# Kernel tuning notes

Measured on AMD Instinct MI355X. Metric: run time of the kernel, lower is better.

## Reference

```python
import jax, jax.numpy as jnp
import numpy as np

NUM_HEADS = 16
MEMORY_LR = 0.1


def setup_inputs() -> dict:
    key = jax.random.key(0)
    ks = jax.random.split(key, 5)
    B, S, D = 4, 4096, 1024
    x = jax.random.normal(ks[0], (B, S, D), dtype=jnp.float32)
    # torch init: randn * 0.01, shape (out_features, in_features)
    Wq = jax.random.normal(ks[1], (D, D), dtype=jnp.float32) * 0.01
    Wk = jax.random.normal(ks[2], (D, D), dtype=jnp.float32) * 0.01
    Wv = jax.random.normal(ks[3], (D, D), dtype=jnp.float32) * 0.01
    Wo = jax.random.normal(ks[4], (D, D), dtype=jnp.float32) * 0.01
    return {"x": x, "Wq": Wq, "Wk": Wk, "Wv": Wv, "Wo": Wo}


def reference(x, Wq, Wk, Wv, Wo):
    B, S, D = x.shape
    H = NUM_HEADS
    hd = D // H
    # Projections (torch Linear: y = x @ W^T). Pending self-mod updates
    # (immediate_update=False) never change W during forward -> plain matmul.
    Q = (x @ Wq.T).reshape(B, S, H, hd)
    K = (x @ Wk.T).reshape(B, S, H, hd)
    V = (x @ Wv.T).reshape(B, S, H, hd)
    # time-major for scan: [S, B, H, hd]
    Qt = jnp.transpose(Q, (1, 0, 2, 3))
    Kt = jnp.transpose(K, (1, 0, 2, 3))
    Vt = jnp.transpose(V, (1, 0, 2, 3))

    def step(M, qkv):
        q, k, v = qkv  # each [B, H, hd]
        v_pred = jnp.einsum('hdk,bhk->bhd', M, k)
        err = v - v_pred
        # torch computes the update under no_grad -> constant w.r.t. params
        upd = jax.lax.stop_gradient(jnp.einsum('bhd,bhk->hdk', err, k) / B)
        M_new = M + MEMORY_LR * upd
        out = jnp.einsum('hdk,bhk->bhd', M_new, q)
        return M_new, out

    M0 = jnp.zeros((H, hd, hd), dtype=x.dtype)  # memory buffer starts at zero
    _, outs = jax.lax.scan(step, M0, (Qt, Kt, Vt))  # outs: [S, B, H, hd]
    out = jnp.transpose(outs, (1, 0, 2, 3)).reshape(B, S, D)
    # dropout p=0.0 -> identity
    return out @ Wo.T
```

## Files before the change

### kernel.cpp

```cpp
#include <hip/hip_runtime.h>


typedef unsigned short u16;
typedef __attribute__((ext_vector_type(8))) short short8;
typedef __attribute__((ext_vector_type(4))) float f32x4;

#define B_ 4
#define S_ 4096
#define D_ 1024
#define H_ 16
#define CHUNK 16
#define NCHUNK 256
#define SUPW 16
#define NSUP 16
#define ETA 0.025f

__device__ __forceinline__ u16 f2bf(float f) {
  unsigned u = __builtin_bit_cast(unsigned, f);
  u += 0x7fffu + ((u >> 16) & 1u);
  return (u16)(u >> 16);
}
__device__ __forceinline__ float bf2f(u16 s) {
  unsigned u = ((unsigned)s) << 16;
  return __builtin_bit_cast(float, u);
}
__device__ __forceinline__ float ldv(float v) { return v; }
__device__ __forceinline__ float ldv(u16 v) { return bf2f(v); }
__device__ __forceinline__ void stv(float* p, float v) { *p = v; }
__device__ __forceinline__ void stv(u16* p, float v) { *p = f2bf(v); }

#define MFMA __builtin_amdgcn_mfma_f32_16x16x32_bf16

__device__ __forceinline__ void gload16(const void* g, void* l) {
  __builtin_amdgcn_global_load_lds(
      (__attribute__((address_space(1))) void*)g,
      (__attribute__((address_space(3))) void*)l, 16, 0, 0);
}

__global__ void cvt_hi_kernel(const float* __restrict__ x, u16* __restrict__ hi, int n4) {
  int i = blockIdx.x * blockDim.x + threadIdx.x;
  int stride = gridDim.x * blockDim.x;
  for (; i < n4; i += stride) {
    float4 v = ((const float4*)x)[i];
    ushort4 h;
    h.x = f2bf(v.x); h.y = f2bf(v.y); h.z = f2bf(v.z); h.w = f2bf(v.w);
    ((ushort4*)hi)[i] = h;
  }
}

__global__ void cvt_hi4_kernel(const float* __restrict__ a, const float* __restrict__ b,
                               const float* __restrict__ c, const float* __restrict__ d,
                               u16* __restrict__ o, int n4) {
  const float* src = (blockIdx.y == 0) ? a : (blockIdx.y == 1) ? b
                   : (blockIdx.y == 2) ? c : d;
  u16* dst = o + (size_t)blockIdx.y * 1048576u;
  int i = blockIdx.x * blockDim.x + threadIdx.x;
  int stride = gridDim.x * blockDim.x;
  for (; i < n4; i += stride) {
    float4 v = ((const float4*)src)[i];
    ushort4 h;
    h.x = f2bf(v.x); h.y = f2bf(v.y); h.z = f2bf(v.z); h.w = f2bf(v.w);
    ((ushort4*)dst)[i] = h;
  }
}

template<int BPRE, typename OutT>
__global__ __launch_bounds__(256) void gemm_axw(
    const u16* __restrict__ Ahg, const void* __restrict__ Bhp,
    OutT* __restrict__ C, int M, int N, int K) {
  __shared__ __align__(16) u16 Ahs[2][128][32];
  __shared__ __align__(16) u16 Bhs[2][128][32];
  const int tid = threadIdx.x, w = tid >> 6, lane = tid & 63;
  const int bm = blockIdx.x * 128, bn = blockIdx.y * 128;
  const int wm = (w >> 1) * 64, wn = (w & 1) * 64;
  const int fr = lane & 15, kb = lane >> 4;
  const int lrow = lane >> 2, lcol = (lane & 3) * 8;

  auto stage = [&](int buf, int k0) {
    {
      const size_t rb = (size_t)(bm + w * 32 + lrow) * K + k0 + lcol;
      gload16(Ahg + rb, &Ahs[buf][w * 32][0]);
      gload16(Ahg + rb + (size_t)16 * K, &Ahs[buf][w * 32 + 16][0]);
    }
    if constexpr (BPRE) {
      const u16* Bhg = (const u16*)Bhp;
      const size_t rb = (size_t)(bn + w * 32 + lrow) * K + k0 + lcol;
      gload16(Bhg + rb, &Bhs[buf][w * 32][0]);
      gload16(Bhg + rb + (size_t)16 * K, &Bhs[buf][w * 32 + 16][0]);
    } else {
      const float* Bm = (const float*)Bhp;
#pragma unroll
      for (int i2 = 0; i2 < 4; ++i2) {
        int e = tid + i2 * 256, r = e >> 3, sg = (e & 7) * 4;
        float4 v = *(const float4*)(&Bm[(size_t)(bn + r) * K + k0 + sg]);
        ushort4 hq;
        hq.x = f2bf(v.x); hq.y = f2bf(v.y); hq.z = f2bf(v.z); hq.w = f2bf(v.w);
        *(ushort4*)(&Bhs[buf][r][sg]) = hq;
      }
    }
  };
  auto compute = [&](int buf, f32x4 (*acc)[4]) {
    short8 ah[4], bh[4];
#pragma unroll
    for (int mi = 0; mi < 4; ++mi)
      ah[mi] = *(const short8*)(&Ahs[buf][wm + mi * 16 + fr][kb * 8]);
#pragma unroll
    for (int ni = 0; ni < 4; ++ni)
      bh[ni] = *(const short8*)(&Bhs[buf][wn + ni * 16 + fr][kb * 8]);
#pragma unroll
    for (int mi = 0; mi < 4; ++mi)
#pragma unroll
      for (int ni = 0; ni < 4; ++ni)
        acc[mi][ni] = MFMA(ah[mi], bh[ni], acc[mi][ni], 0, 0, 0);
  };

  f32x4 acc[4][4];
#pragma unroll
  for (int i = 0; i < 4; ++i)
#pragma unroll
    for (int j = 0; j < 4; ++j) acc[i][j] = (f32x4){0.f, 0.f, 0.f, 0.f};

  const int nt = K >> 5;
  stage(0, 0);
  asm volatile("s_waitcnt vmcnt(0)" ::: "memory");
  __syncthreads();
  int cur = 0;
  for (int t = 0; t < nt; ++t) {
    if (t + 1 < nt) stage(cur ^ 1, (t + 1) * 32);
    compute(cur, acc);
    asm volatile("s_waitcnt vmcnt(0)" ::: "memory");
    __syncthreads();
    cur ^= 1;
  }
  const int fc = lane & 15, fr4 = (lane >> 4) * 4;
#pragma unroll
  for (int mi = 0; mi < 4; ++mi)
#pragma unroll
    for (int ni = 0; ni < 4; ++ni) {
      int gm = bm + wm + mi * 16 + fr4;
      int gn = bn + wn + ni * 16 + fc;
#pragma unroll
      for (int rg = 0; rg < 4; ++rg)
        stv(&C[(size_t)(gm + rg) * N + gn], acc[mi][ni][rg]);
    }
}

template<typename PT>
__global__ __launch_bounds__(256) void phase1_kernel(
    float* __restrict__ Qg, const u16* __restrict__ Kg, u16* __restrict__ Vg,
    PT* __restrict__ Pg, PT* __restrict__ Rg) {
  __shared__ __align__(16) u16 Ks[64][72];
  __shared__ __align__(16) u16 KsT[64][72];
  __shared__ __align__(16) u16 Gh[64][72];
  __shared__ __align__(16) u16 Gl[64][72];
  __shared__ __align__(16) float Ut[64][68];
  __shared__ __align__(16) float Wt[64][68];

  const int c = blockIdx.x, h = blockIdx.y, tid = threadIdx.x;
  const int w = tid >> 6, lane = tid & 63;
  const int fr = lane & 15, kq = lane >> 4, orow = kq * 4;
  const int xr = 16 * w + fr;

  auto gidx = [&](int r, int d) -> size_t {
    return ((size_t)(r & 3) * S_ + (size_t)c * CHUNK + (r >> 2)) * D_ + h * 64 + d;
  };
  auto ldb = [&](const u16 (*M)[72], int row, int s) -> short8 {
    return *(const short8*)(&M[row][32 * s + 8 * kq]);
  };
  auto ldf = [&](const float (*M)[68], int row, int s, short8& hh, short8& ll) {
    const float* p = &M[row][32 * s + 8 * kq];
#pragma unroll
    for (int j = 0; j < 8; ++j) {
      float v = p[j];
      u16 hb = f2bf(v);
      hh[j] = (short)hb;
      ll[j] = (short)f2bf(v - bf2f(hb));
    }
  };
  auto ldfh = [&](const float (*M)[68], int row, int s) -> short8 {
    const float* p = &M[row][32 * s + 8 * kq];
    short8 hh;
#pragma unroll
    for (int j = 0; j < 8; ++j) hh[j] = (short)f2bf(p[j]);
    return hh;
  };

  for (int i = tid; i < 4096; i += 256) {
    int r = i >> 6, d = i & 63;
    size_t g = gidx(r, d);
    u16 kraw = Kg[g];
    Ks[r][d] = kraw;
    KsT[d][r] = kraw;
    Wt[d][r] = ETA * bf2f(kraw);
    Ut[d][r] = ETA * bf2f(Vg[g]);
  }
  __syncthreads();

  f32x4 gacc[4];
#pragma unroll
  for (int ni = 0; ni < 4; ++ni) gacc[ni] = (f32x4){0.f, 0.f, 0.f, 0.f};
  {
    short8 xf[2];
#pragma unroll
    for (int s = 0; s < 2; ++s) xf[s] = ldb(Ks, xr, s);
#pragma unroll
    for (int ni = 0; ni < 4; ++ni)
#pragma unroll
      for (int s = 0; s < 2; ++s)
        gacc[ni] = MFMA(xf[s], ldb(Ks, 16 * ni + fr, s), gacc[ni], 0, 0, 0);
  }

  float sreg[4][4];
  {
    short8 xh[2], xl[2];
#pragma unroll
    for (int s = 0; s < 2; ++s) {
      const float* qp = &Qg[gidx(xr, 32 * s + 8 * kq)];
#pragma unroll
      for (int j = 0; j < 8; ++j) {
        float v = qp[j];
        u16 hb = f2bf(v);
        xh[s][j] = (short)hb;
        xl[s][j] = (short)f2bf(v - bf2f(hb));
      }
    }
    f32x4 acc[4];
#pragma unroll
    for (int ni = 0; ni < 4; ++ni) acc[ni] = (f32x4){0.f, 0.f, 0.f, 0.f};
#pragma unroll
    for (int ni = 0; ni < 4; ++ni)
#pragma unroll
      for (int s = 0; s < 2; ++s) {
        short8 yf = ldb(Ks, 16 * ni + fr, s);
        acc[ni] = MFMA(xh[s], yf, acc[ni], 0, 0, 0);
        acc[ni] = MFMA(xl[s], yf, acc[ni], 0, 0, 0);
      }
#pragma unroll
    for (int ni = 0; ni < 4; ++ni)
#pragma unroll
      for (int rg = 0; rg < 4; ++rg) {
        int r = 16 * w + orow + rg, cc = 16 * ni + fr;
        sreg[ni][rg] = ((r >> 2) >= (cc >> 2)) ? acc[ni][rg] : 0.f;
      }
  }
  __syncthreads();

#pragma unroll
  for (int ni = 0; ni < 4; ++ni)
#pragma unroll
    for (int rg = 0; rg < 4; ++rg) {
      float v = -ETA * gacc[ni][rg];
      u16 hb = f2bf(v);
      u16 lb = f2bf(v - bf2f(hb));
      int rr = 16 * w + orow + rg, cc = 16 * ni + fr;
      bool low = (rr >> 2) > (cc >> 2);
      u16 hm = low ? hb : (u16)0, lm = low ? lb : (u16)0;
      Gh[rr][cc] = hm;
      Gl[rr][cc] = lm;
      Ks[cc][rr] = hm;
    }
  __syncthreads();

  {
    short8 uh[2], ul[2], wh[2], wl[2];
#pragma unroll
    for (int s = 0; s < 2; ++s) { ldf(Ut, xr, s, uh[s], ul[s]); ldf(Wt, xr, s, wh[s], wl[s]); }
    f32x4 aU[4], aW[4];
#pragma unroll
    for (int ni = 0; ni < 4; ++ni) { aU[ni] = (f32x4){0.f,0.f,0.f,0.f}; aW[ni] = (f32x4){0.f,0.f,0.f,0.f}; }
#pragma unroll
    for (int ni = 0; ni < 4; ++ni)
#pragma unroll
      for (int s = 0; s < 2; ++s) {
        short8 yh = ldb(Gh, 16 * ni + fr, s);
        short8 yl = ldb(Gl, 16 * ni + fr, s);
        aU[ni] = MFMA(uh[s], yh, aU[ni], 0, 0, 0);
        aU[ni] = MFMA(uh[s], yl, aU[ni], 0, 0, 0);
        aU[ni] = MFMA(ul[s], yh, aU[ni], 0, 0, 0);
        aW[ni] = MFMA(wh[s], yh, aW[ni], 0, 0, 0);
        aW[ni] = MFMA(wh[s], yl, aW[ni], 0, 0, 0);
        aW[ni] = MFMA(wl[s], yh, aW[ni], 0, 0, 0);
      }
#pragma unroll
    for (int ni = 0; ni < 4; ++ni)
#pragma unroll
      for (int rg = 0; rg < 4; ++rg) {
        Ut[16 * w + orow + rg][16 * ni + fr] += aU[ni][rg];
        Wt[16 * w + orow + rg][16 * ni + fr] += aW[ni][rg];
      }
  }
  auto appSf = [&](const u16 (*Np)[72]) {
    short8 xu[2], xw[2];
#pragma unroll
    for (int s = 0; s < 2; ++s) { xu[s] = ldfh(Ut, xr, s); xw[s] = ldfh(Wt, xr, s); }
    f32x4 aU[4], aW[4];
#pragma unroll
    for (int ni = 0; ni < 4; ++ni) { aU[ni] = (f32x4){0.f,0.f,0.f,0.f}; aW[ni] = (f32x4){0.f,0.f,0.f,0.f}; }
#pragma unroll
    for (int ni = 0; ni < 4; ++ni)
#pragma unroll
      for (int s = 0; s < 2; ++s) {
        short8 yf = ldb(Np, 16 * ni + fr, s);
        aU[ni] = MFMA(xu[s], yf, aU[ni], 0, 0, 0);
        aW[ni] = MFMA(xw[s], yf, aW[ni], 0, 0, 0);
      }
#pragma unroll
    for (int ni = 0; ni < 4; ++ni)
#pragma unroll
      for (int rg = 0; rg < 4; ++rg) {
        Ut[16 * w + orow + rg][16 * ni + fr] += aU[ni][rg];
        Wt[16 * w + orow + rg][16 * ni + fr] += aW[ni][rg];
      }
  };

  {
    f32x4 sq[4];
#pragma unroll
    for (int ni = 0; ni < 4; ++ni) sq[ni] = (f32x4){0.f, 0.f, 0.f, 0.f};
    short8 xh[2];
#pragma unroll
    for (int s = 0; s < 2; ++s) xh[s] = ldb(Gh, xr, s);
#pragma unroll
    for (int ni = 0; ni < 4; ++ni)
#pragma unroll
      for (int s = 0; s < 2; ++s)
        sq[ni] = MFMA(xh[s], ldb(Ks, 16 * ni + fr, s), sq[ni], 0, 0, 0);
    __syncthreads();
#pragma unroll
    for (int ni = 0; ni < 4; ++ni)
#pragma unroll
      for (int rg = 0; rg < 4; ++rg) {
        u16 b = f2bf(sq[ni][rg]);
        int rr = 16 * w + orow + rg, cc = 16 * ni + fr;
        Ks[rr][cc] = b;
        Gh[cc][rr] = b;
      }
  }
  __syncthreads();

  appSf(Ks);
  {
    f32x4 sq[4];
#pragma unroll
    for (int ni = 0; ni < 4; ++ni) sq[ni] = (f32x4){0.f, 0.f, 0.f, 0.f};
    short8 xf[2];
#pragma unroll
    for (int s = 0; s < 2; ++s) xf[s] = ldb(Ks, xr, s);
#pragma unroll
    for (int ni = 0; ni < 4; ++ni)
#pragma unroll
      for (int s = 0; s < 2; ++s)
        sq[ni] = MFMA(xf[s], ldb(Gh, 16 * ni + fr, s), sq[ni], 0, 0, 0);
    __syncthreads();
#pragma unroll
    for (int ni = 0; ni < 4; ++ni)
#pragma unroll
      for (int rg = 0; rg < 4; ++rg) {
        u16 b = f2bf(sq[ni][rg]);
        int rr = 16 * w + orow + rg, cc = 16 * ni + fr;
        Gl[rr][cc] = b;
        Ks[cc][rr] = b;
      }
  }
  __syncthreads();

  appSf(Gl);
  {
    f32x4 sq[4];
#pragma unroll
    for (int ni = 0; ni < 4; ++ni) sq[ni] = (f32x4){0.f, 0.f, 0.f, 0.f};
    short8 xf[2];
#pragma unroll
    for (int s = 0; s < 2; ++s) xf[s] = ldb(Gl, xr, s);
#pragma unroll
    for (int ni = 0; ni < 4; ++ni)
#pragma unroll
      for (int s = 0; s < 2; ++s)
        sq[ni] = MFMA(xf[s], ldb(Ks, 16 * ni + fr, s), sq[ni], 0, 0, 0);
#pragma unroll
    for (int ni = 0; ni < 4; ++ni)
#pragma unroll
      for (int rg = 0; rg < 4; ++rg)
        Gh[16 * w + orow + rg][16 * ni + fr] = f2bf(sq[ni][rg]);
  }
  __syncthreads();

  appSf(Gh);
  __syncthreads();

  const size_t base = ((size_t)c * H_ + h) * 4096;
  {
    short8 wh[2], wl[2], uh[2], ul[2];
#pragma unroll
    for (int s = 0; s < 2; ++s) { ldf(Wt, xr, s, wh[s], wl[s]); ldf(Ut, xr, s, uh[s], ul[s]); }
    f32x4 aP[4], aR[4];
#pragma unroll
    for (int ni = 0; ni < 4; ++ni) { aP[ni] = (f32x4){0.f,0.f,0.f,0.f}; aR[ni] = (f32x4){0.f,0.f,0.f,0.f}; }
#pragma unroll
    for (int ni = 0; ni < 4; ++ni)
#pragma unroll
      for (int s = 0; s < 2; ++s) {
        short8 yf = ldb(KsT, 16 * ni + fr, s);
        aP[ni] = MFMA(wh[s], yf, aP[ni], 0, 0, 0);
        aP[ni] = MFMA(wl[s], yf, aP[ni], 0, 0, 0);
        aR[ni] = MFMA(uh[s], yf, aR[ni], 0, 0, 0);
        aR[ni] = MFMA(ul[s], yf, aR[ni], 0, 0, 0);
      }
#pragma unroll
    for (int ni = 0; ni < 4; ++ni)
#pragma unroll
      for (int rg = 0; rg < 4; ++rg) {
        stv(&Pg[base + (16 * w + orow + rg) * 64 + 16 * ni + fr], aP[ni][rg]);
        stv(&Rg[base + (16 * w + orow + rg) * 64 + 16 * ni + fr], aR[ni][rg]);
      }
  }
  {
    const int r = tid >> 2, d0 = (tid & 3) * 16;
    short8 v0, v1;
#pragma unroll
    for (int j = 0; j < 8; ++j) v0[j] = (short)f2bf(Wt[r][d0 + j]);
#pragma unroll
    for (int j = 0; j < 8; ++j) v1[j] = (short)f2bf(Wt[r][d0 + 8 + j]);
    *(short8*)(&Gh[r][d0]) = v0;
    *(short8*)(&Gh[r][d0 + 8]) = v1;
#pragma unroll
    for (int j = 0; j < 8; ++j) v0[j] = (short)f2bf(Ut[r][d0 + j]);
#pragma unroll
    for (int j = 0; j < 8; ++j) v1[j] = (short)f2bf(Ut[r][d0 + 8 + j]);
    *(short8*)(&Gl[r][d0]) = v0;
    *(short8*)(&Gl[r][d0 + 8]) = v1;
  }
#pragma unroll
  for (int ni = 0; ni < 4; ++ni)
#pragma unroll
    for (int rg = 0; rg < 4; ++rg)
      Ks[16 * w + orow + rg][16 * ni + fr] = f2bf(sreg[ni][rg]);
  __syncthreads();

  {
    short8 xs[2];
#pragma unroll
    for (int s = 0; s < 2; ++s) xs[s] = ldb(Ks, xr, s);
    f32x4 accE[4], accF[4];
#pragma unroll
    for (int ni = 0; ni < 4; ++ni) {
      accE[ni] = (f32x4){0.f, 0.f, 0.f, 0.f};
      accF[ni] = (f32x4){0.f, 0.f, 0.f, 0.f};
    }
#pragma unroll
    for (int ni = 0; ni < 4; ++ni)
#pragma unroll
      for (int s = 0; s < 2; ++s) {
        accE[ni] = MFMA(xs[s], ldb(Gh, 16 * ni + fr, s), accE[ni], 0, 0, 0);
        accF[ni] = MFMA(xs[s], ldb(Gl, 16 * ni + fr, s), accF[ni], 0, 0, 0);
      }
#pragma unroll
    for (int ni = 0; ni < 4; ++ni)
#pragma unroll
      for (int rg = 0; rg < 4; ++rg) {
        int r = 16 * w + orow + rg, d = 16 * ni + fr;
        size_t g = gidx(r, d);
        float qv = Qg[g];
        Qg[g] = qv - accE[ni][rg];
        Vg[g] = f2bf(accF[ni][rg]);
      }
  }
}

__device__ __forceinline__ void store64(float* dst, const float (*src)[65], int tid) {
  for (int i = tid; i < 4096; i += 256) dst[i] = src[i >> 6][i & 63];
}
__device__ __forceinline__ void mm64(const float (*X)[65], const float (*Y)[65],
                                     float (*Dst)[65], const float (*Add)[65], int tid) {
  const int r0 = (tid >> 4) * 4, c0 = (tid & 15) * 4;
  float a[4][4] = {};
  for (int d = 0; d < 64; ++d) {
    float xv[4], yv[4];
#pragma unroll
    for (int i = 0; i < 4; ++i) xv[i] = X[r0 + i][d];
#pragma unroll
    for (int j = 0; j < 4; ++j) yv[j] = Y[d][c0 + j];
#pragma unroll
    for (int i = 0; i < 4; ++i)
#pragma unroll
      for (int j = 0; j < 4; ++j) a[i][j] += xv[i] * yv[j];
  }
  __syncthreads();
#pragma unroll
  for (int i = 0; i < 4; ++i)
#pragma unroll
    for (int j = 0; j < 4; ++j) {
      float v = a[i][j];
      if (Add) v += Add[r0 + i][c0 + j];
      Dst[r0 + i][c0 + j] = v;
    }
  __syncthreads();
}

template<typename PT>
__global__ __launch_bounds__(256) void seq_levelA(const PT* __restrict__ Pg,
    const PT* __restrict__ Rg, float* __restrict__ Psup, float* __restrict__ Rsup) {
  __shared__ __align__(16) float Pa[64][68], Ra[64][68], Ri[64][68];
  __shared__ __align__(16) u16 Pih[64][72], Pil[64][72];
  const int sup = blockIdx.x, h = blockIdx.y, tid = threadIdx.x;
  const int w = tid >> 6, lane = tid & 63;
  const int fr = lane & 15, kq = lane >> 4, orow = kq * 4;
  const int xr = 16 * w + fr;
  const int cbase = sup * SUPW;

  auto upd = [&](float (*St)[68], const float (*Add)[68]) {
    short8 xh[2], xl[2];
#pragma unroll
    for (int s2 = 0; s2 < 2; ++s2) {
      const float* p = &St[xr][32 * s2 + 8 * kq];
#pragma unroll
      for (int j = 0; j < 8; ++j) {
        float v = p[j];
        u16 hb = f2bf(v);
        xh[s2][j] = (short)hb;
        xl[s2][j] = (short)f2bf(v - bf2f(hb));
      }
    }
    f32x4 acc[4];
#pragma unroll
    for (int ni = 0; ni < 4; ++ni) acc[ni] = (f32x4){0.f, 0.f, 0.f, 0.f};
#pragma unroll
    for (int ni = 0; ni < 4; ++ni)
#pragma unroll
      for (int s2 = 0; s2 < 2; ++s2) {
        short8 yh = *(const short8*)(&Pih[16 * ni + fr][32 * s2 + 8 * kq]);
        short8 yl = *(const short8*)(&Pil[16 * ni + fr][32 * s2 + 8 * kq]);
        acc[ni] = MFMA(xh[s2], yh, acc[ni], 0, 0, 0);
        acc[ni] = MFMA(xh[s2], yl, acc[ni], 0, 0, 0);
        acc[ni] = MFMA(xl[s2], yh, acc[ni], 0, 0, 0);
      }
#pragma unroll
    for (int ni = 0; ni < 4; ++ni)
#pragma unroll
      for (int rg = 0; rg < 4; ++rg) {
        float v = acc[ni][rg];
        if (Add) v += Add[16 * w + orow + rg][16 * ni + fr];
        St[16 * w + orow + rg][16 * ni + fr] = v;
      }
  };

  {
    const PT* ps = Pg + ((size_t)cbase * H_ + h) * 4096;
    const PT* rs = Rg + ((size_t)cbase * H_ + h) * 4096;
    for (int i = tid; i < 4096; i += 256) {
      int r = i >> 6, cc = i & 63;
      Pa[r][cc] = ((r == cc) ? 1.f : 0.f) - ldv(ps[i]);
      Ra[r][cc] = ldv(rs[i]);
    }
  }
  float pf[16], rf[16];
  {
    const PT* ps = Pg + ((size_t)(cbase + 1) * H_ + h) * 4096;
    const PT* rs = Rg + ((size_t)(cbase + 1) * H_ + h) * 4096;
#pragma unroll
    for (int k = 0; k < 16; ++k) { int i = tid + k * 256; pf[k] = ldv(ps[i]); rf[k] = ldv(rs[i]); }
  }
  for (int s = 1; s < SUPW; ++s) {
#pragma unroll
    for (int k = 0; k < 16; ++k) {
      int i = tid + k * 256, d = i >> 6, cc = i & 63;
      float v = ((d == cc) ? 1.f : 0.f) - pf[k];
      u16 hb = f2bf(v);
      Pih[cc][d] = hb;
      Pil[cc][d] = f2bf(v - bf2f(hb));
      Ri[d][cc] = rf[k];
    }
    __syncthreads();
    if (s + 1 < SUPW) {
      const PT* ps = Pg + ((size_t)(cbase + s + 1) * H_ + h) * 4096;
      const PT* rs = Rg + ((size_t)(cbase + s + 1) * H_ + h) * 4096;
#pragma unroll
      for (int k = 0; k < 16; ++k) { int i = tid + k * 256; pf[k] = ldv(ps[i]); rf[k] = ldv(rs[i]); }
    }
    upd(Pa, nullptr);
    upd(Ra, Ri);
    __syncthreads();
  }
  for (int i = tid; i < 4096; i += 256) {
    Psup[((size_t)sup * H_ + h) * 4096 + i] = Pa[i >> 6][i & 63];
    Rsup[((size_t)sup * H_ + h) * 4096 + i] = Ra[i >> 6][i & 63];
  }
}

__global__ __launch_bounds__(256) void seq_levelB(const float* __restrict__ Psup,
    const float* __restrict__ Rsup, float* __restrict__ Msup) {
  __shared__ float Ms[64][65], Pi[64][65], Ri[64][65];
  const int h = blockIdx.x, tid = threadIdx.x;
  for (int i = tid; i < 4096; i += 256) Ms[i >> 6][i & 63] = 0.f;
  float pf[16], rf[16];
  {
    const float* ps = Psup + ((size_t)0 * H_ + h) * 4096;
    const float* rs = Rsup + ((size_t)0 * H_ + h) * 4096;
#pragma unroll
    for (int k = 0; k < 16; ++k) { int i = tid + k * 256; pf[k] = ps[i]; rf[k] = rs[i]; }
  }
  for (int s = 0; s < NSUP; ++s) {
#pragma unroll
    for (int k = 0; k < 16; ++k) {
      int i = tid + k * 256, r = i >> 6, cc = i & 63;
      Pi[r][cc] = pf[k];
      Ri[r][cc] = rf[k];
    }
    store64(Msup + ((size_t)s * H_ + h) * 4096, Ms, tid);
    __syncthreads();
    if (s + 1 < NSUP) {
      const float* ps = Psup + ((size_t)(s + 1) * H_ + h) * 4096;
      const float* rs = Rsup + ((size_t)(s + 1) * H_ + h) * 4096;
#pragma unroll
      for (int k = 0; k < 16; ++k) { int i = tid + k * 256; pf[k] = ps[i]; rf[k] = rs[i]; }
    }
    mm64(Ms, Pi, Ms, Ri, tid);
  }
}

template<typename PT>
__global__ __launch_bounds__(256) void seq_levelC(const PT* __restrict__ Pg,
    PT* __restrict__ Rg, const float* __restrict__ Msup) {
  __shared__ __align__(16) float Ms[64][68], Ri[64][68];
  __shared__ __align__(16) u16 Pih[64][72], Pil[64][72];
  const int sup = blockIdx.x, h = blockIdx.y, tid = threadIdx.x;
  const int w = tid >> 6, lane = tid & 63;
  const int fr = lane & 15, kq = lane >> 4, orow = kq * 4;
  const int xr = 16 * w + fr;

  auto upd = [&](float (*St)[68], const float (*Add)[68]) {
    short8 xh[2], xl[2];
#pragma unroll
    for (int s2 = 0; s2 < 2; ++s2) {
      const float* p = &St[xr][32 * s2 + 8 * kq];
#pragma unroll
      for (int j = 0; j < 8; ++j) {
        float v = p[j];
        u16 hb = f2bf(v);
        xh[s2][j] = (short)hb;
        xl[s2][j] = (short)f2bf(v - bf2f(hb));
      }
    }
    f32x4 acc[4];
#pragma unroll
    for (int ni = 0; ni < 4; ++ni) acc[ni] = (f32x4){0.f, 0.f, 0.f, 0.f};
#pragma unroll
    for (int ni = 0; ni < 4; ++ni)
#pragma unroll
      for (int s2 = 0; s2 < 2; ++s2) {
        short8 yh = *(const short8*)(&Pih[16 * ni + fr][32 * s2 + 8 * kq]);
        short8 yl = *(const short8*)(&Pil[16 * ni + fr][32 * s2 + 8 * kq]);
        acc[ni] = MFMA(xh[s2], yh, acc[ni], 0, 0, 0);
        acc[ni] = MFMA(xh[s2], yl, acc[ni], 0, 0, 0);
        acc[ni] = MFMA(xl[s2], yh, acc[ni], 0, 0, 0);
      }
#pragma unroll
    for (int ni = 0; ni < 4; ++ni)
#pragma unroll
      for (int rg = 0; rg < 4; ++rg) {
        float v = acc[ni][rg];
        if (Add) v += Add[16 * w + orow + rg][16 * ni + fr];
        St[16 * w + orow + rg][16 * ni + fr] = v;
      }
  };

  for (int i = tid; i < 4096; i += 256)
    Ms[i >> 6][i & 63] = Msup[((size_t)sup * H_ + h) * 4096 + i];
  float pf[16], rf[16];
  {
    const size_t slice = ((size_t)(sup * SUPW) * H_ + h) * 4096;
#pragma unroll
    for (int k = 0; k < 16; ++k) { int i = tid + k * 256; pf[k] = ldv(Pg[slice + i]); rf[k] = ldv(Rg[slice + i]); }
  }
  for (int s = 0; s < SUPW; ++s) {
    const size_t slice = ((size_t)(sup * SUPW + s) * H_ + h) * 4096;
#pragma unroll
    for (int k = 0; k < 16; ++k) {
      int i = tid + k * 256, d = i >> 6, cc = i & 63;
      float v = ((d == cc) ? 1.f : 0.f) - pf[k];
      u16 hb = f2bf(v);
      Pih[cc][d] = hb;
      Pil[cc][d] = f2bf(v - bf2f(hb));
      Ri[d][cc] = rf[k];
    }
    for (int i = tid; i < 4096; i += 256) stv(&Rg[slice + i], Ms[i >> 6][i & 63]);
    __syncthreads();
    if (s + 1 < SUPW) {
      const size_t sl2 = ((size_t)(sup * SUPW + s + 1) * H_ + h) * 4096;
#pragma unroll
      for (int k = 0; k < 16; ++k) { int i = tid + k * 256; pf[k] = ldv(Pg[sl2 + i]); rf[k] = ldv(Rg[sl2 + i]); }
    }
    upd(Ms, Ri);
    __syncthreads();
  }
}

template<typename PT>
__global__ __launch_bounds__(256) void phase3_kernel(
    const float* __restrict__ Eg, const u16* __restrict__ Fg,
    const PT* __restrict__ Mcg, u16* __restrict__ attn) {
  __shared__ float Es[64][65], Ms[64][65];
  const int c = blockIdx.x, h = blockIdx.y, tid = threadIdx.x;
  for (int i = tid; i < 4096; i += 256) {
    int r = i >> 6, d = i & 63, t = r >> 2, b = r & 3;
    size_t g = ((size_t)b * S_ + (size_t)c * CHUNK + t) * D_ + h * 64 + d;
    Es[r][d] = Eg[g];
    Ms[i >> 6][i & 63] = ldv(Mcg[((size_t)c * H_ + h) * 4096 + i]);
  }
  __syncthreads();
  const int r0 = (tid >> 4) * 4, d0 = (tid & 15) * 4;
  float a[4][4] = {};
  for (int k = 0; k < 64; ++k) {
    float ev[4], mv[4];
#pragma unroll
    for (int i = 0; i < 4; ++i) ev[i] = Es[r0 + i][k];
#pragma unroll
    for (int j = 0; j < 4; ++j) mv[j] = Ms[d0 + j][k];
#pragma unroll
    for (int i = 0; i < 4; ++i)
#pragma unroll
      for (int j = 0; j < 4; ++j) a[i][j] += ev[i] * mv[j];
  }
#pragma unroll
  for (int i = 0; i < 4; ++i)
#pragma unroll
    for (int j = 0; j < 4; ++j) {
      int r = r0 + i, d = d0 + j, t = r >> 2, b = r & 3;
      size_t g = ((size_t)b * S_ + (size_t)c * CHUNK + t) * D_ + h * 64 + d;
      attn[g] = f2bf(a[i][j] + bf2f(Fg[g]));
    }
}

extern "C" void kernel_launch(void* const* d_in, const int* in_sizes, int n_in,
                              void* d_out, int out_size, void* d_ws, size_t ws_size,
                              hipStream_t stream) {
  (void)in_sizes; (void)n_in; (void)out_size;
  const float* x  = (const float*)d_in[0];
  const float* Wq = (const float*)d_in[1];
  const float* Wk = (const float*)d_in[2];
  const float* Wv = (const float*)d_in[3];
  const float* Wo = (const float*)d_in[4];
  float* out = (float*)d_out;

  char* w = (char*)d_ws;
  const size_t MB = 1024 * 1024;
  u16* Kbf = (u16*)w;
  u16* Vbf = (u16*)(w + 32 * MB);
  u16* xh  = (u16*)(w + 64 * MB);
  u16* P   = (u16*)(w + 64 * MB);
  u16* R   = (u16*)(w + 96 * MB);
  float* Psup = (float*)w;
  float* Rsup = (float*)(w + 4 * MB);
  float* Msup = (float*)(w + 8 * MB);
  u16* attn = P;
  u16* Wsp = (u16*)(w + 128 * MB);
  const bool big = ws_size >= 144 * MB;

  const size_t DSZ = (size_t)B_ * S_ * D_;
  cvt_hi_kernel<<<2048, 256, 0, stream>>>(x, xh, (int)(DSZ / 4));

  dim3 gg(128, 8);
  if (big) {
    cvt_hi4_kernel<<<dim3(512, 4), 256, 0, stream>>>(Wq, Wk, Wv, Wo, Wsp, 262144);
    gemm_axw<1, float><<<gg, 256, 0, stream>>>(xh, Wsp + 0 * 1048576u, out, 16384, 1024, 1024);
    gemm_axw<1, u16><<<gg, 256, 0, stream>>>(xh, Wsp + 1 * 1048576u, Kbf, 16384, 1024, 1024);
    gemm_axw<1, u16><<<gg, 256, 0, stream>>>(xh, Wsp + 2 * 1048576u, Vbf, 16384, 1024, 1024);
    phase1_kernel<u16><<<dim3(NCHUNK, H_), 256, 0, stream>>>(out, Kbf, Vbf, P, R);
    seq_levelA<u16><<<dim3(NSUP, H_), 256, 0, stream>>>(P, R, Psup, Rsup);
    seq_levelB<<<dim3(H_), 256, 0, stream>>>(Psup, Rsup, Msup);
    seq_levelC<u16><<<dim3(NSUP, H_), 256, 0, stream>>>(P, R, Msup);
    phase3_kernel<u16><<<dim3(NCHUNK, H_), 256, 0, stream>>>(out, Vbf, R, attn);
    gemm_axw<1, float><<<gg, 256, 0, stream>>>(attn, Wsp + 3 * 1048576u, out, 16384, 1024, 1024);
  } else {
    gemm_axw<0, float><<<gg, 256, 0, stream>>>(xh, Wq, out, 16384, 1024, 1024);
    gemm_axw<0, u16><<<gg, 256, 0, stream>>>(xh, Wk, Kbf, 16384, 1024, 1024);
    gemm_axw<0, u16><<<gg, 256, 0, stream>>>(xh, Wv, Vbf, 16384, 1024, 1024);
    phase1_kernel<u16><<<dim3(NCHUNK, H_), 256, 0, stream>>>(out, Kbf, Vbf, P, R);
    seq_levelA<u16><<<dim3(NSUP, H_), 256, 0, stream>>>(P, R, Psup, Rsup);
    seq_levelB<<<dim3(H_), 256, 0, stream>>>(Psup, Rsup, Msup);
    seq_levelC<u16><<<dim3(NSUP, H_), 256, 0, stream>>>(P, R, Msup);
    phase3_kernel<u16><<<dim3(NCHUNK, H_), 256, 0, stream>>>(out, Vbf, R, attn);
    gemm_axw<0, float><<<gg, 256, 0, stream>>>(attn, Wo, out, 16384, 1024, 1024);
  }
}
```

Measured before the change: 538.3 us.

## Fuse phase3 output computation into seq_levelC and drop chunk-state writeback

The per-chunk output product E·M^T plus the F correction is now computed inside seq_levelC with split-bf16 MFMA while the running memory state sits in shared memory. This removes the writeback of per-chunk states into R, the separate phase3 launch, and its reload of those states. The result is written in place into the V buffer, which then feeds the output projection. The cost is that the output work now runs inside a sequential scan with only 256 blocks, adding loads, MFMAs and an extra barrier per step.

```diff
diff --git a/kernel.cpp b/kernel.cpp
--- a/kernel.cpp
+++ b/kernel.cpp
@@ -620,27 +620,33 @@
 
 template<typename PT>
 __global__ __launch_bounds__(256) void seq_levelC(const PT* __restrict__ Pg,
-    PT* __restrict__ Rg, const float* __restrict__ Msup) {
-  __shared__ __align__(16) float Ms[64][68], Ri[64][68];
+    const PT* __restrict__ Rg, const float* __restrict__ Msup,
+    const float* __restrict__ Eg, u16* __restrict__ FAg) {
+  __shared__ __align__(16) float Ms[64][68], Ri[64][68], Es[64][68];
   __shared__ __align__(16) u16 Pih[64][72], Pil[64][72];
   const int sup = blockIdx.x, h = blockIdx.y, tid = threadIdx.x;
   const int w = tid >> 6, lane = tid & 63;
   const int fr = lane & 15, kq = lane >> 4, orow = kq * 4;
   const int xr = 16 * w + fr;
 
+  auto gidx = [&](int c, int r, int d) -> size_t {
+    return ((size_t)(r & 3) * S_ + (size_t)c * CHUNK + (r >> 2)) * D_ + h * 64 + d;
+  };
+  auto ldf = [&](const float (*M)[68], int row, int s2, short8& hh, short8& ll) {
+    const float* p = &M[row][32 * s2 + 8 * kq];
+#pragma unroll
+    for (int j = 0; j < 8; ++j) {
+      float v = p[j];
+      u16 hb = f2bf(v);
+      hh[j] = (short)hb;
+      ll[j] = (short)f2bf(v - bf2f(hb));
+    }
+  };
+
   auto upd = [&](float (*St)[68], const float (*Add)[68]) {
     short8 xh[2], xl[2];
 #pragma unroll
-    for (int s2 = 0; s2 < 2; ++s2) {
-      const float* p = &St[xr][32 * s2 + 8 * kq];
-#pragma unroll
-      for (int j = 0; j < 8; ++j) {
-        float v = p[j];
-        u16 hb = f2bf(v);
-        xh[s2][j] = (short)hb;
-        xl[s2][j] = (short)f2bf(v - bf2f(hb));
-      }
-    }
+    for (int s2 = 0; s2 < 2; ++s2) ldf(St, xr, s2, xh[s2], xl[s2]);
     f32x4 acc[4];
 #pragma unroll
     for (int ni = 0; ni < 4; ++ni) acc[ni] = (f32x4){0.f, 0.f, 0.f, 0.f};
@@ -666,14 +672,20 @@
 
   for (int i = tid; i < 4096; i += 256)
     Ms[i >> 6][i & 63] = Msup[((size_t)sup * H_ + h) * 4096 + i];
-  float pf[16], rf[16];
+  float pf[16], rf[16], ef[16];
   {
     const size_t slice = ((size_t)(sup * SUPW) * H_ + h) * 4096;
-#pragma unroll
-    for (int k = 0; k < 16; ++k) { int i = tid + k * 256; pf[k] = ldv(Pg[slice + i]); rf[k] = ldv(Rg[slice + i]); }
+    const int c0 = sup * SUPW;
+#pragma unroll
+    for (int k = 0; k < 16; ++k) {
+      int i = tid + k * 256;
+      pf[k] = ldv(Pg[slice + i]);
+      rf[k] = ldv(Rg[slice + i]);
+      ef[k] = Eg[gidx(c0, i >> 6, i & 63)];
+    }
   }
   for (int s = 0; s < SUPW; ++s) {
-    const size_t slice = ((size_t)(sup * SUPW + s) * H_ + h) * 4096;
+    const int c = sup * SUPW + s;
 #pragma unroll
     for (int k = 0; k < 16; ++k) {
       int i = tid + k * 256, d = i >> 6, cc = i & 63;
@@ -682,53 +694,49 @@
       Pih[cc][d] = hb;
       Pil[cc][d] = f2bf(v - bf2f(hb));
       Ri[d][cc] = rf[k];
-    }
-    for (int i = tid; i < 4096; i += 256) stv(&Rg[slice + i], Ms[i >> 6][i & 63]);
+      Es[d][cc] = ef[k];
+    }
     __syncthreads();
     if (s + 1 < SUPW) {
-      const size_t sl2 = ((size_t)(sup * SUPW + s + 1) * H_ + h) * 4096;
-#pragma unroll
-      for (int k = 0; k < 16; ++k) { int i = tid + k * 256; pf[k] = ldv(Pg[sl2 + i]); rf[k] = ldv(Rg[sl2 + i]); }
-    }
+      const size_t sl2 = ((size_t)(c + 1) * H_ + h) * 4096;
+#pragma unroll
+      for (int k = 0; k < 16; ++k) {
+        int i = tid + k * 256;
+        pf[k] = ldv(Pg[sl2 + i]);
+        rf[k] = ldv(Rg[sl2 + i]);
+        ef[k] = Eg[gidx(c + 1, i >> 6, i & 63)];
+      }
+    }
+    {
+      short8 exh[2], exl[2];
+#pragma unroll
+      for (int s2 = 0; s2 < 2; ++s2) ldf(Es, xr, s2, exh[s2], exl[s2]);
+      f32x4 at[4];
+#pragma unroll
+      for (int ni = 0; ni < 4; ++ni) at[ni] = (f32x4){0.f, 0.f, 0.f, 0.f};
+#pragma unroll
+      for (int ni = 0; ni < 4; ++ni)
+#pragma unroll
+        for (int s2 = 0; s2 < 2; ++s2) {
+          short8 yh, yl;
+          ldf(Ms, 16 * ni + fr, s2, yh, yl);
+          at[ni] = MFMA(exh[s2], yh, at[ni], 0, 0, 0);
+          at[ni] = MFMA(exh[s2], yl, at[ni], 0, 0, 0);
+          at[ni] = MFMA(exl[s2], yh, at[ni], 0, 0, 0);
+        }
+#pragma unroll
+      for (int ni = 0; ni < 4; ++ni)
+#pragma unroll
+        for (int rg = 0; rg < 4; ++rg) {
+          int r = 16 * w + orow + rg, d = 16 * ni + fr;
+          size_t g = gidx(c, r, d);
+          FAg[g] = f2bf(at[ni][rg] + bf2f(FAg[g]));
+        }
+    }
+    __syncthreads();
     upd(Ms, Ri);
     __syncthreads();
   }
-}
-
-template<typename PT>
-__global__ __launch_bounds__(256) void phase3_kernel(
-    const float* __restrict__ Eg, const u16* __restrict__ Fg,
-    const PT* __restrict__ Mcg, u16* __restrict__ attn) {
-  __shared__ float Es[64][65], Ms[64][65];
-  const int c = blockIdx.x, h = blockIdx.y, tid = threadIdx.x;
-  for (int i = tid; i < 4096; i += 256) {
-    int r = i >> 6, d = i & 63, t = r >> 2, b = r & 3;
-    size_t g = ((size_t)b * S_ + (size_t)c * CHUNK + t) * D_ + h * 64 + d;
-    Es[r][d] = Eg[g];
-    Ms[i >> 6][i & 63] = ldv(Mcg[((size_t)c * H_ + h) * 4096 + i]);
-  }
-  __syncthreads();
-  const int r0 = (tid >> 4) * 4, d0 = (tid & 15) * 4;
-  float a[4][4] = {};
-  for (int k = 0; k < 64; ++k) {
-    float ev[4], mv[4];
-#pragma unroll
-    for (int i = 0; i < 4; ++i) ev[i] = Es[r0 + i][k];
-#pragma unroll
-    for (int j = 0; j < 4; ++j) mv[j] = Ms[d0 + j][k];
-#pragma unroll
-    for (int i = 0; i < 4; ++i)
-#pragma unroll
-      for (int j = 0; j < 4; ++j) a[i][j] += ev[i] * mv[j];
-  }
-#pragma unroll
-  for (int i = 0; i < 4; ++i)
-#pragma unroll
-    for (int j = 0; j < 4; ++j) {
-      int r = r0 + i, d = d0 + j, t = r >> 2, b = r & 3;
-      size_t g = ((size_t)b * S_ + (size_t)c * CHUNK + t) * D_ + h * 64 + d;
-      attn[g] = f2bf(a[i][j] + bf2f(Fg[g]));
-    }
 }
 
 extern "C" void kernel_launch(void* const* d_in, const int* in_sizes, int n_in,
@@ -752,7 +760,6 @@
   float* Psup = (float*)w;
   float* Rsup = (float*)(w + 4 * MB);
   float* Msup = (float*)(w + 8 * MB);
-  u16* attn = P;
   u16* Wsp = (u16*)(w + 128 * MB);
   const bool big = ws_size >= 144 * MB;
 
@@ -768,9 +775,8 @@
     phase1_kernel<u16><<<dim3(NCHUNK, H_), 256, 0, stream>>>(out, Kbf, Vbf, P, R);
     seq_levelA<u16><<<dim3(NSUP, H_), 256, 0, stream>>>(P, R, Psup, Rsup);
     seq_levelB<<<dim3(H_), 256, 0, stream>>>(Psup, Rsup, Msup);
-    seq_levelC<u16><<<dim3(NSUP, H_), 256, 0, stream>>>(P, R, Msup);
-    phase3_kernel<u16><<<dim3(NCHUNK, H_), 256, 0, stream>>>(out, Vbf, R, attn);
-    gemm_axw<1, float><<<gg, 256, 0, stream>>>(attn, Wsp + 3 * 1048576u, out, 16384, 1024, 1024);
+    seq_levelC<u16><<<dim3(NSUP, H_), 256, 0, stream>>>(P, R, Msup, out, Vbf);
+    gemm_axw<1, float><<<gg, 256, 0, stream>>>(Vbf, Wsp + 3 * 1048576u, out, 16384, 1024, 1024);
   } else {
     gemm_axw<0, float><<<gg, 256, 0, stream>>>(xh, Wq, out, 16384, 1024, 1024);
     gemm_axw<0, u16><<<gg, 256, 0, stream>>>(xh, Wk, Kbf, 16384, 1024, 1024);
@@ -778,8 +784,7 @@
     phase1_kernel<u16><<<dim3(NCHUNK, H_), 256, 0, stream>>>(out, Kbf, Vbf, P, R);
     seq_levelA<u16><<<dim3(NSUP, H_), 256, 0, stream>>>(P, R, Psup, Rsup);
     seq_levelB<<<dim3(H_), 256, 0, stream>>>(Psup, Rsup, Msup);
-    seq_levelC<u16><<<dim3(NSUP, H_), 256, 0, stream>>>(P, R, Msup);
-    phase3_kernel<u16><<<dim3(NCHUNK, H_), 256, 0, stream>>>(out, Vbf, R, attn);
-    gemm_axw<0, float><<<gg, 256, 0, stream>>>(attn, Wo, out, 16384, 1024, 1024);
-  }
-}
+    seq_levelC<u16><<<dim3(NSUP, H_), 256, 0, stream>>>(P, R, Msup, out, Vbf);
+    gemm_axw<0, float><<<gg, 256, 0, stream>>>(Vbf, Wo, out, 16384, 1024, 1024);
+  }
+}
```

New measurement: 524.8 us. 2.5% less time.
